# Kernel optimization log

Measured on AMD Instinct MI355X. Metric: run time of the kernel, lower is better.

Reference implementation:

```python
import jax, jax.numpy as jnp
import numpy as np

E = 600000
N = 50000
H = 128
OE = 256


def swish(v):
    return v * jax.nn.sigmoid(v)


def setup_inputs() -> dict:
    key = jax.random.key(0)
    ks = jax.random.split(key, 16)
    inp = {
        "x": jax.random.normal(ks[0], (E, H), dtype=jnp.float32),
        "rbf": jax.random.normal(ks[1], (E, 6), dtype=jnp.float32),
        "i": jax.random.randint(ks[2], (E,), 0, N, dtype=jnp.int32),
        "edge_index": jax.random.randint(ks[3], (2, E), 0, N, dtype=jnp.int32),
        "edge_weight": jax.random.uniform(ks[4], (E,), dtype=jnp.float32),
        "batch": jax.random.randint(ks[5], (N,), 0, 32, dtype=jnp.int32),
        "num_nodes": N,
        "W_rbf": jax.random.normal(ks[6], (H, 6), dtype=jnp.float32) * 0.2,
        "W_up": jax.random.normal(ks[7], (OE, H), dtype=jnp.float32) * (1.0 / np.sqrt(H)),
        "b_up": jnp.zeros((OE,), dtype=jnp.float32),
        "W_l1": jax.random.normal(ks[8], (OE, OE), dtype=jnp.float32) * (1.0 / np.sqrt(OE)),
        "b_l1": jnp.zeros((OE,), dtype=jnp.float32),
        "W_l2": jax.random.normal(ks[9], (OE, OE), dtype=jnp.float32) * (1.0 / np.sqrt(OE)),
        "b_l2": jnp.zeros((OE,), dtype=jnp.float32),
        "W_l3": jax.random.normal(ks[10], (OE, OE), dtype=jnp.float32) * (1.0 / np.sqrt(OE)),
        "b_l3": jnp.zeros((OE,), dtype=jnp.float32),
        "W_out": jax.random.normal(ks[11], (1, OE), dtype=jnp.float32) * (1.0 / np.sqrt(OE)),
        "W_w": jax.random.normal(ks[12], (1, H), dtype=jnp.float32) * (1.0 / np.sqrt(H)),
        "b_w": jnp.zeros((1,), dtype=jnp.float32),
    }
    return inp


def reference(x, rbf, i, edge_index, edge_weight, batch, num_nodes,
              W_rbf, W_up, b_up, W_l1, b_l1, W_l2, b_l2, W_l3, b_l3,
              W_out, W_w, b_w):
    # edge_index / edge_weight are unused in the original forward.
    # x = lin_rbf(rbf) * x  -> [E, H]
    xe = (rbf @ W_rbf.T) * x
    # scatter-add edges -> nodes: [N, H]
    xn = jax.ops.segment_sum(xe, i, num_segments=num_nodes)
    # energy head: alpha = w_lin(x) before lin_up
    alpha = xn @ W_w.T + b_w  # [N, 1]
    x2 = xn @ W_up.T + b_up   # [N, OE]
    for W, b in ((W_l1, b_l1), (W_l2, b_l2), (W_l3, b_l3)):
        x2 = swish(x2 @ W.T + b)
    out = (x2 @ W_out.T) * alpha  # [N, 1]
    return (out, batch)
```

## Files before the change

kernel.cpp:

```cpp
#include <hip/hip_runtime.h>
#include <hip/hip_bf16.h>
#include <math.h>

#define E_CNT 600000
#define N_CNT 50000
#define H_DIM 128
#define OE_DIM 256

typedef __attribute__((ext_vector_type(8))) short short8;
typedef __attribute__((ext_vector_type(4))) float f32x4;

#define WS_OFF    0
#define WS_CURS   200008
#define WS_CNT    400008
#define WS_TEXC   600008
#define WS_BSUM   800712
#define WS_WUP    801736
#define WS_WL1    867272
#define WS_WL2    998344
#define WS_WL3    1129416
#define WS_XE     1261568

#define SCAN_NB 196
#define WCONV_NB 896

__global__ __launch_bounds__(256) void histwconv_kernel(
    const int* __restrict__ nid, int* __restrict__ counts,
    const float* __restrict__ Wup, const float* __restrict__ Wl1,
    const float* __restrict__ Wl2, const float* __restrict__ Wl3,
    ushort* __restrict__ dUp, ushort* __restrict__ dL1,
    ushort* __restrict__ dL2, ushort* __restrict__ dL3)
{
    if (blockIdx.x < WCONV_NB) {
        int d = blockIdx.x * 256 + threadIdx.x;
        const float* W;
        ushort* dst;
        int K;
        if (d < 32768)       { W = Wup; dst = dUp; K = 128; }
        else if (d < 98304)  { d -= 32768;  W = Wl1; dst = dL1; K = 256; }
        else if (d < 163840) { d -= 98304;  W = Wl2; dst = dL2; K = 256; }
        else                 { d -= 163840; W = Wl3; dst = dL3; K = 256; }
        int j = d & 7;
        int l = (d >> 3) & 63;
        int KS = K >> 5;
        int ks = (d >> 9) % KS;
        int ot = (d >> 9) / KS;
        int k = ks * 32 + ((l >> 4) << 3) + j;
        int o = ot * 16 + (l & 15);
        __hip_bfloat16 h = __float2bfloat16(W[o * K + k]);
        dst[d] = *(const ushort*)&h;
    } else {
        int nb = gridDim.x - WCONV_NB;
        for (int e = (blockIdx.x - WCONV_NB) * 256 + threadIdx.x; e < E_CNT;
             e += nb * 256)
            atomicAdd(&counts[nid[e]], 1);
    }
}

__global__ __launch_bounds__(256) void scanA_kernel(const int* __restrict__ counts,
                                                    int* __restrict__ texc,
                                                    int* __restrict__ bsum)
{
    __shared__ int s[256];
    const int t = threadIdx.x;
    const int i = blockIdx.x * 256 + t;
    int v = (i < N_CNT) ? counts[i] : 0;
    s[t] = v;
    __syncthreads();
    for (int off = 1; off < 256; off <<= 1) {
        int u = (t >= off) ? s[t - off] : 0;
        __syncthreads();
        s[t] += u;
        __syncthreads();
    }
    texc[i] = s[t] - v;
    if (t == 255) bsum[blockIdx.x] = s[255];
}

__global__ __launch_bounds__(256) void scanC_kernel(const int* __restrict__ texc,
                                                    const int* __restrict__ bsum,
                                                    int* __restrict__ offs,
                                                    int* __restrict__ cursor)
{
    __shared__ int red[256];
    const int t = threadIdx.x;
    int v = (t < (int)blockIdx.x && t < SCAN_NB) ? bsum[t] : 0;
    red[t] = v;
    __syncthreads();
    for (int off = 128; off >= 1; off >>= 1) {
        if (t < off) red[t] += red[t + off];
        __syncthreads();
    }
    const int boff = red[0];
    const int i = blockIdx.x * 256 + t;
    if (i < N_CNT) {
        int o = texc[i] + boff;
        offs[i] = o;
        cursor[i] = o;
    }
    if (i == 0) offs[N_CNT] = E_CNT;
}

__global__ __launch_bounds__(256, 4) void prepass_kernel(
    const float* __restrict__ x, const float* __restrict__ rbf,
    const int* __restrict__ nid, int* __restrict__ cursor,
    const float* __restrict__ W_rbf,
    ushort* __restrict__ xep)
{
    const int tid = threadIdx.x;
    const int lane = tid & 63;
    const int half = lane >> 5;
    const int l31 = lane & 31;
    const int h0 = l31 * 4;

    float wrb[4][6];
#pragma unroll
    for (int j = 0; j < 4; ++j)
#pragma unroll
        for (int k = 0; k < 6; ++k)
            wrb[j][k] = W_rbf[(h0 + j) * 6 + k];

    const int wid = (blockIdx.x * 256 + tid) >> 6;
    const int nw = (gridDim.x * 256) >> 6;
    const int npair = E_CNT / 2;

    for (int p = wid; p < npair; p += nw) {
        const int e = p * 2 + half;
        const int node = nid[e];
        int slot = 0;
        if (l31 == 0) slot = atomicAdd(&cursor[node], 1);
        slot = __shfl(slot, half << 5);

        const float4 xv = *(const float4*)(x + (size_t)e * H_DIM + h0);
        const float2* rp = (const float2*)(rbf + (size_t)e * 6);
        const float2 q0 = rp[0], q1 = rp[1], q2 = rp[2];
        const float r[6] = {q0.x, q0.y, q1.x, q1.y, q2.x, q2.y};
        float c0 = 0.f, c1 = 0.f, c2 = 0.f, c3 = 0.f;
#pragma unroll
        for (int k = 0; k < 6; ++k) {
            c0 = fmaf(r[k], wrb[0][k], c0);
            c1 = fmaf(r[k], wrb[1][k], c1);
            c2 = fmaf(r[k], wrb[2][k], c2);
            c3 = fmaf(r[k], wrb[3][k], c3);
        }
        const float v0 = c0 * xv.x, v1 = c1 * xv.y, v2 = c2 * xv.z, v3 = c3 * xv.w;
        __hip_bfloat16 b0 = __float2bfloat16(v0), b1 = __float2bfloat16(v1);
        __hip_bfloat16 b2 = __float2bfloat16(v2), b3 = __float2bfloat16(v3);
        ushort4 pk;
        pk.x = *(const ushort*)&b0;
        pk.y = *(const ushort*)&b1;
        pk.z = *(const ushort*)&b2;
        pk.w = *(const ushort*)&b3;
        *(ushort4*)(xep + (size_t)slot * H_DIM + h0) = pk;
    }
}

#define MB 32
#define PITCH 264

template<int KS, bool SW>
__device__ __forceinline__ void layer(const ushort* __restrict__ Wsh,
                                      const float* __restrict__ bias,
                                      const ushort* in_s, ushort* out_s, int tid)
{
    const int w = tid >> 6, lane = tid & 63;
    const int l15 = lane & 15, lg = lane >> 4;

    f32x4 acc[2][2];
#pragma unroll
    for (int mi = 0; mi < 2; ++mi)
#pragma unroll
        for (int oi = 0; oi < 2; ++oi)
            acc[mi][oi] = (f32x4){0.f, 0.f, 0.f, 0.f};

#pragma unroll
    for (int ks = 0; ks < KS; ++ks) {
        short8 b0 = *(const short8*)(Wsh + (size_t)(((w * 2 + 0) * KS + ks) * 64 + lane) * 8);
        short8 b1 = *(const short8*)(Wsh + (size_t)(((w * 2 + 1) * KS + ks) * 64 + lane) * 8);
#pragma unroll
        for (int mi = 0; mi < 2; ++mi) {
            short8 a = *(const short8*)(in_s + (mi * 16 + l15) * PITCH + ks * 32 + lg * 8);
            acc[mi][0] = __builtin_amdgcn_mfma_f32_16x16x32_bf16(a, b0, acc[mi][0], 0, 0, 0);
            acc[mi][1] = __builtin_amdgcn_mfma_f32_16x16x32_bf16(a, b1, acc[mi][1], 0, 0, 0);
        }
    }

#pragma unroll
    for (int oi = 0; oi < 2; ++oi) {
        float bv = bias[(w * 2 + oi) * 16 + l15];
#pragma unroll
        for (int mi = 0; mi < 2; ++mi)
#pragma unroll
            for (int r = 0; r < 4; ++r) {
                float v = acc[mi][oi][r] + bv;
                if (SW) v = v / (1.f + __expf(-v));
                __hip_bfloat16 h = __float2bfloat16(v);
                out_s[(mi * 16 + lg * 4 + r) * PITCH + (w * 2 + oi) * 16 + l15] =
                    *(const ushort*)&h;
            }
    }
}

__global__ __launch_bounds__(512, 6) void fused_kernel(
    const ushort* __restrict__ xep,
    const int* __restrict__ offs,
    const float* __restrict__ W_w, const float* __restrict__ b_w,
    const ushort* __restrict__ Wup, const ushort* __restrict__ Wl1,
    const ushort* __restrict__ Wl2, const ushort* __restrict__ Wl3,
    const float* __restrict__ b_up, const float* __restrict__ b_l1,
    const float* __restrict__ b_l2, const float* __restrict__ b_l3,
    const float* __restrict__ W_out, const int* __restrict__ batch,
    float* __restrict__ out)
{
    __shared__ ushort sA[MB * PITCH];
    __shared__ ushort sB[MB * PITCH];
    __shared__ int s_off[MB + 1];
    __shared__ float s_alpha[MB];

    const int tid = threadIdx.x;
    const int w = tid >> 6, lane = tid & 63;
    const int node0 = blockIdx.x * MB;

    if (tid < MB) {
        int node = node0 + tid;
        if (node < N_CNT) out[N_CNT + node] = (float)batch[node];
    }
    if (tid < MB + 1)
        s_off[tid] = offs[min(node0 + tid, N_CNT)];
    __syncthreads();

    {
        const int eq = lane >> 4;
        const int p = lane & 15;
        float ww[8];
#pragma unroll
        for (int j = 0; j < 8; ++j) ww[j] = W_w[p * 8 + j];
        const float bw = b_w[0];

        for (int nl4 = 0; nl4 < 4; ++nl4) {
            const int nl = (w << 2) + nl4;
            const int ls = s_off[nl], le = s_off[nl + 1];
            float acc[8];
#pragma unroll
            for (int j = 0; j < 8; ++j) acc[j] = 0.f;

#pragma unroll 2
            for (int s = ls + eq; s < le; s += 4) {
                short8 rv = *(const short8*)(xep + (size_t)s * H_DIM + p * 8);
#pragma unroll
                for (int j = 0; j < 8; ++j) {
                    ushort u = (ushort)rv[j];
                    acc[j] += __bfloat162float(*(const __hip_bfloat16*)&u);
                }
            }
#pragma unroll
            for (int j = 0; j < 8; ++j) {
                acc[j] += __shfl_xor(acc[j], 16);
                acc[j] += __shfl_xor(acc[j], 32);
            }
            float part = 0.f;
#pragma unroll
            for (int j = 0; j < 8; ++j) part = fmaf(acc[j], ww[j], part);
            part += __shfl_xor(part, 1);
            part += __shfl_xor(part, 2);
            part += __shfl_xor(part, 4);
            part += __shfl_xor(part, 8);
            if (lane == 0) s_alpha[nl] = part + bw;
            if (eq == 0) {
                ushort pk[8];
#pragma unroll
                for (int j = 0; j < 8; ++j) {
                    __hip_bfloat16 h = __float2bfloat16(acc[j]);
                    pk[j] = *(const ushort*)&h;
                }
                *(int4*)(sA + nl * PITCH + p * 8) = *(const int4*)pk;
            }
        }
    }
    __syncthreads();

    layer<4, false>(Wup, b_up, sA, sB, tid);
    __syncthreads();
    layer<8, true>(Wl1, b_l1, sB, sA, tid);
    __syncthreads();
    layer<8, true>(Wl2, b_l2, sA, sB, tid);
    __syncthreads();
    layer<8, true>(Wl3, b_l3, sB, sA, tid);
    __syncthreads();

    {
        int nl = tid >> 4, q = tid & 15;
        const ushort* rowp = sA + nl * PITCH + q * 16;
        float sum = 0.f;
#pragma unroll
        for (int o = 0; o < 16; ++o) {
            __hip_bfloat16 h = *(const __hip_bfloat16*)(rowp + o);
            sum = fmaf(__bfloat162float(h), W_out[q * 16 + o], sum);
        }
        sum += __shfl_xor(sum, 1);
        sum += __shfl_xor(sum, 2);
        sum += __shfl_xor(sum, 4);
        sum += __shfl_xor(sum, 8);
        int node = node0 + nl;
        if (q == 0 && node < N_CNT) out[node] = sum * s_alpha[nl];
    }
}

extern "C" void kernel_launch(void* const* d_in, const int* in_sizes, int n_in,
                              void* d_out, int out_size, void* d_ws, size_t ws_size,
                              hipStream_t stream)
{
    const float* x      = (const float*)d_in[0];
    const float* rbf    = (const float*)d_in[1];
    const int*   nid    = (const int*)d_in[2];
    const int*   batch  = (const int*)d_in[5];
    const float* W_rbf  = (const float*)d_in[7];
    const float* W_up   = (const float*)d_in[8];
    const float* b_up   = (const float*)d_in[9];
    const float* W_l1   = (const float*)d_in[10];
    const float* b_l1   = (const float*)d_in[11];
    const float* W_l2   = (const float*)d_in[12];
    const float* b_l2   = (const float*)d_in[13];
    const float* W_l3   = (const float*)d_in[14];
    const float* b_l3   = (const float*)d_in[15];
    const float* W_out  = (const float*)d_in[16];
    const float* W_w    = (const float*)d_in[17];
    const float* b_w    = (const float*)d_in[18];

    char* ws = (char*)d_ws;
    int*    offs   = (int*)(ws + WS_OFF);
    int*    cursor = (int*)(ws + WS_CURS);
    int*    counts = (int*)(ws + WS_CNT);
    int*    texc   = (int*)(ws + WS_TEXC);
    int*    bsum   = (int*)(ws + WS_BSUM);
    ushort* WupS   = (ushort*)(ws + WS_WUP);
    ushort* Wl1S   = (ushort*)(ws + WS_WL1);
    ushort* Wl2S   = (ushort*)(ws + WS_WL2);
    ushort* Wl3S   = (ushort*)(ws + WS_WL3);
    ushort* xep    = (ushort*)(ws + WS_XE);
    float*  out    = (float*)d_out;

    hipMemsetAsync(counts, 0, N_CNT * sizeof(int), stream);
    histwconv_kernel<<<WCONV_NB + 1024, 256, 0, stream>>>(
        nid, counts, W_up, W_l1, W_l2, W_l3, WupS, Wl1S, Wl2S, Wl3S);
    scanA_kernel<<<SCAN_NB, 256, 0, stream>>>(counts, texc, bsum);
    scanC_kernel<<<SCAN_NB, 256, 0, stream>>>(texc, bsum, offs, cursor);

    prepass_kernel<<<2048, 256, 0, stream>>>(x, rbf, nid, cursor, W_rbf, xep);

    fused_kernel<<<(N_CNT + MB - 1) / MB, 512, 0, stream>>>(
        xep, offs, W_w, b_w,
        WupS, Wl1S, Wl2S, Wl3S, b_up, b_l1, b_l2, b_l3, W_out, batch, out);
}
```

Measured before the change: 219.7 us.

## Record per-edge rank in histogram pass and drop cursor atomics in prepass

The histogram pass now stores the return value of its atomic increment as a per-edge rank, so the prepass computes each edge's destination slot as offs[node]+rank with no atomics. This removes the second round of contended atomics on the cursor array and the shuffle needed to broadcast the slot. The prepass is also reshaped so each wave handles four edges with 16 lanes each, loading 8 floats per lane and writing 16-byte packed bf16 stores. The cost is an extra 2.4 MB rank array that is written once and read once.

```diff
diff --git a/kernel.cpp b/kernel.cpp
--- a/kernel.cpp
+++ b/kernel.cpp
@@ -11,21 +11,22 @@
 typedef __attribute__((ext_vector_type(4))) float f32x4;
 
 #define WS_OFF    0
-#define WS_CURS   200008
-#define WS_CNT    400008
-#define WS_TEXC   600008
-#define WS_BSUM   800712
-#define WS_WUP    801736
-#define WS_WL1    867272
-#define WS_WL2    998344
-#define WS_WL3    1129416
-#define WS_XE     1261568
+#define WS_CNT    200016
+#define WS_TEXC   400016
+#define WS_BSUM   600720
+#define WS_WUP    601744
+#define WS_WL1    667280
+#define WS_WL2    798352
+#define WS_WL3    929424
+#define WS_RANK   1060496
+#define WS_XE     3460496
 
 #define SCAN_NB 196
 #define WCONV_NB 896
 
 __global__ __launch_bounds__(256) void histwconv_kernel(
     const int* __restrict__ nid, int* __restrict__ counts,
+    int* __restrict__ rank,
     const float* __restrict__ Wup, const float* __restrict__ Wl1,
     const float* __restrict__ Wl2, const float* __restrict__ Wl3,
     ushort* __restrict__ dUp, ushort* __restrict__ dL1,
@@ -53,7 +54,7 @@
         int nb = gridDim.x - WCONV_NB;
         for (int e = (blockIdx.x - WCONV_NB) * 256 + threadIdx.x; e < E_CNT;
              e += nb * 256)
-            atomicAdd(&counts[nid[e]], 1);
+            rank[e] = atomicAdd(&counts[nid[e]], 1);
     }
 }
 
@@ -79,8 +80,7 @@
 
 __global__ __launch_bounds__(256) void scanC_kernel(const int* __restrict__ texc,
                                                     const int* __restrict__ bsum,
-                                                    int* __restrict__ offs,
-                                                    int* __restrict__ cursor)
+                                                    int* __restrict__ offs)
 {
     __shared__ int red[256];
     const int t = threadIdx.x;
@@ -93,65 +93,59 @@
     }
     const int boff = red[0];
     const int i = blockIdx.x * 256 + t;
-    if (i < N_CNT) {
-        int o = texc[i] + boff;
-        offs[i] = o;
-        cursor[i] = o;
-    }
+    if (i < N_CNT) offs[i] = texc[i] + boff;
     if (i == 0) offs[N_CNT] = E_CNT;
 }
 
 __global__ __launch_bounds__(256, 4) void prepass_kernel(
     const float* __restrict__ x, const float* __restrict__ rbf,
-    const int* __restrict__ nid, int* __restrict__ cursor,
-    const float* __restrict__ W_rbf,
+    const int* __restrict__ nid, const int* __restrict__ rank,
+    const int* __restrict__ offs, const float* __restrict__ W_rbf,
     ushort* __restrict__ xep)
 {
     const int tid = threadIdx.x;
     const int lane = tid & 63;
-    const int half = lane >> 5;
-    const int l31 = lane & 31;
-    const int h0 = l31 * 4;
-
-    float wrb[4][6];
-#pragma unroll
-    for (int j = 0; j < 4; ++j)
+    const int q = lane >> 4;
+    const int p = lane & 15;
+    const int h0 = p * 8;
+
+    float wrb[8][6];
+#pragma unroll
+    for (int j = 0; j < 8; ++j)
 #pragma unroll
         for (int k = 0; k < 6; ++k)
             wrb[j][k] = W_rbf[(h0 + j) * 6 + k];
 
     const int wid = (blockIdx.x * 256 + tid) >> 6;
     const int nw = (gridDim.x * 256) >> 6;
-    const int npair = E_CNT / 2;
-
-    for (int p = wid; p < npair; p += nw) {
-        const int e = p * 2 + half;
-        const int node = nid[e];
-        int slot = 0;
-        if (l31 == 0) slot = atomicAdd(&cursor[node], 1);
-        slot = __shfl(slot, half << 5);
-
-        const float4 xv = *(const float4*)(x + (size_t)e * H_DIM + h0);
+    const int nquad = E_CNT / 4;
+
+    for (int t = wid; t < nquad; t += nw) {
+        const int e = t * 4 + q;
+        const int slot = offs[nid[e]] + rank[e];
+
+        const float4 xa = *(const float4*)(x + (size_t)e * H_DIM + h0);
+        const float4 xb = *(const float4*)(x + (size_t)e * H_DIM + h0 + 4);
         const float2* rp = (const float2*)(rbf + (size_t)e * 6);
         const float2 q0 = rp[0], q1 = rp[1], q2 = rp[2];
         const float r[6] = {q0.x, q0.y, q1.x, q1.y, q2.x, q2.y};
-        float c0 = 0.f, c1 = 0.f, c2 = 0.f, c3 = 0.f;
-#pragma unroll
-        for (int k = 0; k < 6; ++k) {
-            c0 = fmaf(r[k], wrb[0][k], c0);
-            c1 = fmaf(r[k], wrb[1][k], c1);
-            c2 = fmaf(r[k], wrb[2][k], c2);
-            c3 = fmaf(r[k], wrb[3][k], c3);
-        }
-        const float v0 = c0 * xv.x, v1 = c1 * xv.y, v2 = c2 * xv.z, v3 = c3 * xv.w;
-        __hip_bfloat16 b0 = __float2bfloat16(v0), b1 = __float2bfloat16(v1);
-        __hip_bfloat16 b2 = __float2bfloat16(v2), b3 = __float2bfloat16(v3);
-        ushort4 pk;
-        pk.x = *(const ushort*)&b0;
-        pk.y = *(const ushort*)&b1;
-        pk.z = *(const ushort*)&b2;
-        pk.w = *(const ushort*)&b3;
-        *(ushort4*)(xep + (size_t)slot * H_DIM + h0) = pk;
+
+        float c[8];
+#pragma unroll
+        for (int j = 0; j < 8; ++j) {
+            float cc = 0.f;
+#pragma unroll
+            for (int k = 0; k < 6; ++k) cc = fmaf(r[k], wrb[j][k], cc);
+            c[j] = cc;
+        }
+        const float xv[8] = {xa.x, xa.y, xa.z, xa.w, xb.x, xb.y, xb.z, xb.w};
+        ushort pk[8];
+#pragma unroll
+        for (int j = 0; j < 8; ++j) {
+            __hip_bfloat16 h = __float2bfloat16(c[j] * xv[j]);
+            pk[j] = *(const ushort*)&h;
+        }
+        *(int4*)(xep + (size_t)slot * H_DIM + h0) = *(const int4*)pk;
     }
 }
 
@@ -329,7 +323,6 @@
 
     char* ws = (char*)d_ws;
     int*    offs   = (int*)(ws + WS_OFF);
-    int*    cursor = (int*)(ws + WS_CURS);
     int*    counts = (int*)(ws + WS_CNT);
     int*    texc   = (int*)(ws + WS_TEXC);
     int*    bsum   = (int*)(ws + WS_BSUM);
@@ -337,16 +330,17 @@
     ushort* Wl1S   = (ushort*)(ws + WS_WL1);
     ushort* Wl2S   = (ushort*)(ws + WS_WL2);
     ushort* Wl3S   = (ushort*)(ws + WS_WL3);
+    int*    rank   = (int*)(ws + WS_RANK);
     ushort* xep    = (ushort*)(ws + WS_XE);
     float*  out    = (float*)d_out;
 
     hipMemsetAsync(counts, 0, N_CNT * sizeof(int), stream);
     histwconv_kernel<<<WCONV_NB + 1024, 256, 0, stream>>>(
-        nid, counts, W_up, W_l1, W_l2, W_l3, WupS, Wl1S, Wl2S, Wl3S);
+        nid, counts, rank, W_up, W_l1, W_l2, W_l3, WupS, Wl1S, Wl2S, Wl3S);
     scanA_kernel<<<SCAN_NB, 256, 0, stream>>>(counts, texc, bsum);
-    scanC_kernel<<<SCAN_NB, 256, 0, stream>>>(texc, bsum, offs, cursor);
-
-    prepass_kernel<<<2048, 256, 0, stream>>>(x, rbf, nid, cursor, W_rbf, xep);
+    scanC_kernel<<<SCAN_NB, 256, 0, stream>>>(texc, bsum, offs);
+
+    prepass_kernel<<<2048, 256, 0, stream>>>(x, rbf, nid, rank, offs, W_rbf, xep);
 
     fused_kernel<<<(N_CNT + MB - 1) / MB, 512, 0, stream>>>(
         xep, offs, W_w, b_w,
```

Result: slower. 233.9 us (+6.5%).
